# Optimization experiments

Hardware: AMD Instinct MI355X
Metric: run time of the kernel (lower is better)

## Reference

```python
import jax, jax.numpy as jnp
import numpy as np

N_NODES = 50000
N_EDGES = 800000
IN_F = 128
OUT_F = 128

def setup_inputs() -> dict:
    key = jax.random.key(0)
    k1, k2, k3, k4, k5, k6 = jax.random.split(key, 6)
    x = jax.random.normal(k1, (N_NODES, IN_F), dtype=jnp.float32)
    edge_row = jax.random.randint(k2, (N_EDGES,), 0, N_NODES, dtype=jnp.int32)
    edge_col = jax.random.randint(k3, (N_EDGES,), 0, N_NODES, dtype=jnp.int32)
    edge_val = jax.random.uniform(k4, (N_EDGES,), dtype=jnp.float32)
    stdv = 1.0 / np.sqrt(OUT_F)
    weight = jax.random.uniform(k5, (IN_F, OUT_F), minval=-stdv, maxval=stdv, dtype=jnp.float32)
    bias_param = jax.random.uniform(k6, (OUT_F,), minval=-stdv, maxval=stdv, dtype=jnp.float32)
    return {"x": x, "edge_row": edge_row, "edge_col": edge_col,
            "edge_val": edge_val, "weight": weight, "bias_param": bias_param}

def reference(x, edge_row, edge_col, edge_val, weight, bias_param):
    # support = X @ W  (dense GEMM)
    support = jnp.matmul(x, weight)                      # [N, out_f]
    # out = spmm(adj, support): gather source rows, scale by edge value,
    # scatter-add into destination rows (COO SpMM)
    msgs = edge_val[:, None] * support[edge_col]         # [E, out_f]
    out = jax.ops.segment_sum(msgs, edge_row, num_segments=N_NODES)
    return out + bias_param
```

## Files before the change

kernel.cpp:

```cpp
#include <hip/hip_runtime.h>

#define IN_F 128
#define OUT_F 128
#define BROWS 64
#define BCAP  2048
#define NBMAX 1024

typedef __attribute__((ext_vector_type(8))) short short8;
typedef __attribute__((ext_vector_type(4))) float floatx4;

__device__ __forceinline__ short f2bf(float f) {
  union { float f; unsigned u; } v; v.f = f;
  unsigned u = v.u;
  unsigned r = (u + 0x7fffu + ((u >> 16) & 1u)) >> 16;
  return (short)r;
}
__device__ __forceinline__ float bflo(unsigned u) { return __uint_as_float(u << 16); }
__device__ __forceinline__ float bfhi(unsigned u) { return __uint_as_float(u & 0xffff0000u); }

__global__ __launch_bounds__(256) void prep_wt(const float* __restrict__ w,
                                               short* __restrict__ wt) {
  int i = blockIdx.x * 256 + threadIdx.x;
  int n = i >> 7, k = i & 127;
  wt[i] = f2bf(w[k * 128 + n]);
}

__global__ __launch_bounds__(256) void gemm_mfma(const float* __restrict__ x,
                                                 const short* __restrict__ wt,
                                                 unsigned short* __restrict__ sup,
                                                 int n) {
  const int w    = threadIdx.x >> 6;
  const int lane = threadIdx.x & 63;
  const int m    = lane & 15;
  const int q    = lane >> 4;
  const int row  = blockIdx.x * 64 + w * 16 + m;

  floatx4 acc[8];
#pragma unroll
  for (int t = 0; t < 8; ++t) acc[t] = (floatx4)(0.f);

#pragma unroll
  for (int kk = 0; kk < 4; ++kk) {
    short8 a;
    if (row < n) {
      const float4* px = (const float4*)(x + (size_t)row * IN_F + kk * 32 + q * 8);
      float4 lo = px[0], hi = px[1];
      a[0] = f2bf(lo.x); a[1] = f2bf(lo.y); a[2] = f2bf(lo.z); a[3] = f2bf(lo.w);
      a[4] = f2bf(hi.x); a[5] = f2bf(hi.y); a[6] = f2bf(hi.z); a[7] = f2bf(hi.w);
    } else {
      a = (short8)(0);
    }
#pragma unroll
    for (int t = 0; t < 8; ++t) {
      short8 b = *(const short8*)(wt + (size_t)(16 * t + m) * 128 + kk * 32 + q * 8);
      acc[t] = __builtin_amdgcn_mfma_f32_16x16x32_bf16(a, b, acc[t], 0, 0, 0);
    }
  }

#pragma unroll
  for (int r = 0; r < 4; ++r) {
    int row_out = blockIdx.x * 64 + w * 16 + q * 4 + r;
    if (row_out < n) {
#pragma unroll
      for (int t = 0; t < 8; ++t) {
        sup[(size_t)row_out * OUT_F + 16 * t + m] = (unsigned short)f2bf(acc[t][r]);
      }
    }
  }
}

__global__ __launch_bounds__(256) void init_cursor(int* __restrict__ cursor, int nb) {
  int b = blockIdx.x * 256 + threadIdx.x;
  if (b < nb) cursor[b] = b * BCAP;
}

__global__ __launch_bounds__(256) void bin_edges(const int* __restrict__ erow,
                                                 const int* __restrict__ ecol,
                                                 const float* __restrict__ eval_,
                                                 int* __restrict__ cursor,
                                                 int2* __restrict__ slab,
                                                 int n_edges, int nb) {
  __shared__ int lhist[NBMAX];
  const int t = threadIdx.x;
  for (int b = t; b < nb; b += 256) lhist[b] = 0;
  __syncthreads();

  const int base = blockIdx.x * 4096;
  int meta[16], col[16]; float val[16];
#pragma unroll
  for (int i = 0; i < 16; ++i) {
    int e = base + i * 256 + t;
    meta[i] = -1;
    if (e < n_edges) {
      int r  = erow[e];
      col[i] = ecol[e];
      val[i] = eval_[e];
      int b = r >> 6, rl = r & 63;
      int rank = atomicAdd(&lhist[b], 1);
      meta[i] = (b << 18) | (rl << 12) | rank;
    }
  }
  __syncthreads();

  for (int b = t; b < nb; b += 256) {
    int c = lhist[b];
    lhist[b] = c ? atomicAdd(&cursor[b], c) : 0;
  }
  __syncthreads();

#pragma unroll
  for (int i = 0; i < 16; ++i) {
    if (meta[i] >= 0) {
      int b = meta[i] >> 18, rl = (meta[i] >> 12) & 63, rank = meta[i] & 0xfff;
      int pos = lhist[b] + rank;
      if (pos < (b + 1) * BCAP)
        slab[pos] = make_int2(col[i] | (rl << 16), __float_as_int(val[i]));
    }
  }
}

__global__ __launch_bounds__(256) void spmm_sorted(const int* __restrict__ cursor,
                                                   const int2* __restrict__ slab,
                                                   const uint4* __restrict__ supv,
                                                   const float* __restrict__ bias,
                                                   float* __restrict__ out,
                                                   int n_nodes) {
  __shared__ int2 srec[BCAP];
  __shared__ int  roff[BROWS + 1];
  __shared__ int  rcur[BROWS];
  const int t = threadIdx.x, b = blockIdx.x;
  const int start = b * BCAP;
  const int cnt = min(cursor[b] - start, BCAP);
  const int w = t >> 6, lane = t & 63;

  if (t < BROWS) rcur[t] = 0;
  __syncthreads();
  for (int i = t; i < cnt; i += 256)
    atomicAdd(&rcur[(slab[start + i].x >> 16) & 63], 1);
  __syncthreads();
  if (w == 0) {
    int inc = rcur[lane];
    #pragma unroll
    for (int d = 1; d < 64; d <<= 1) {
      int u = __shfl_up(inc, d);
      if (lane >= d) inc += u;
    }
    roff[lane + 1] = inc;
    if (lane == 0) roff[0] = 0;
  }
  __syncthreads();
  if (t < BROWS) rcur[t] = roff[t];
  __syncthreads();
  for (int i = t; i < cnt; i += 256) {
    int2 r = slab[start + i];
    int p = atomicAdd(&rcur[(r.x >> 16) & 63], 1);
    srec[p] = r;
  }
  __syncthreads();

  const int g = lane >> 4, s = lane & 15;
  const float4* bp = (const float4*)bias + s * 2;
  const float4 b0 = bp[0], b1 = bp[1];

  for (int it = 0; it < 4; ++it) {
    const int rl = w * 16 + it * 4 + g;
    const int s0 = roff[rl];
    const int c  = roff[rl + 1] - s0;
    int mx = max(c, __shfl_xor(c, 16));
    mx = max(mx, __shfl_xor(mx, 32));

    float a0 = 0.f, a1 = 0.f, a2 = 0.f, a3 = 0.f,
          a4 = 0.f, a5 = 0.f, a6 = 0.f, a7 = 0.f;

    int2 rec0 = make_int2(0, 0), rec1 = make_int2(0, 0);
    if (0 < c) rec0 = srec[s0];
    if (1 < c) rec1 = srec[s0 + 1];
    uint4 sv0 = supv[(size_t)(rec0.x & 0xffff) * 16 + s];
    uint4 sv1 = supv[(size_t)(rec1.x & 0xffff) * 16 + s];

    for (int j = 0; j < mx; ++j) {
      int2 rec2 = make_int2(0, 0);
      if (j + 2 < c) rec2 = srec[s0 + j + 2];
      uint4 sv2 = supv[(size_t)(rec2.x & 0xffff) * 16 + s];
      float v = (j < c) ? __int_as_float(rec0.y) : 0.f;
      a0 = fmaf(v, bflo(sv0.x), a0);
      a1 = fmaf(v, bfhi(sv0.x), a1);
      a2 = fmaf(v, bflo(sv0.y), a2);
      a3 = fmaf(v, bfhi(sv0.y), a3);
      a4 = fmaf(v, bflo(sv0.z), a4);
      a5 = fmaf(v, bfhi(sv0.z), a5);
      a6 = fmaf(v, bflo(sv0.w), a6);
      a7 = fmaf(v, bfhi(sv0.w), a7);
      rec0 = rec1; rec1 = rec2; sv0 = sv1; sv1 = sv2;
    }

    const int row = b * BROWS + rl;
    if (row < n_nodes) {
      float4* op = (float4*)(out + (size_t)row * OUT_F + s * 8);
      op[0] = make_float4(a0 + b0.x, a1 + b0.y, a2 + b0.z, a3 + b0.w);
      op[1] = make_float4(a4 + b1.x, a5 + b1.y, a6 + b1.z, a7 + b1.w);
    }
  }
}

extern "C" void kernel_launch(void* const* d_in, const int* in_sizes, int n_in,
                              void* d_out, int out_size, void* d_ws, size_t ws_size,
                              hipStream_t stream) {
  const float* x     = (const float*)d_in[0];
  const int*   erow  = (const int*)d_in[1];
  const int*   ecol  = (const int*)d_in[2];
  const float* eval_ = (const float*)d_in[3];
  const float* w     = (const float*)d_in[4];
  const float* bias  = (const float*)d_in[5];
  float* out = (float*)d_out;

  const int n_nodes = in_sizes[0] / IN_F;
  const int n_edges = in_sizes[1];
  const int nb = (n_nodes + BROWS - 1) / BROWS;

  char* ws = (char*)d_ws;
  size_t off = 0;
  auto carve = [&](size_t bytes) { void* p = ws + off; off = (off + bytes + 255) & ~(size_t)255; return p; };
  unsigned short* sup = (unsigned short*)carve((size_t)n_nodes * OUT_F * sizeof(unsigned short));
  short* wt           = (short*)carve((size_t)IN_F * OUT_F * sizeof(short));
  int*   cursor       = (int*)  carve((size_t)nb * sizeof(int));
  int2*  slab         = (int2*) carve((size_t)nb * BCAP * sizeof(int2));

  prep_wt<<<(IN_F * OUT_F) / 256, 256, 0, stream>>>(w, wt);
  gemm_mfma<<<(n_nodes + 63) / 64, 256, 0, stream>>>(x, wt, sup, n_nodes);
  init_cursor<<<(nb + 255) / 256, 256, 0, stream>>>(cursor, nb);
  bin_edges<<<(n_edges + 4095) / 4096, 256, 0, stream>>>(erow, ecol, eval_, cursor, slab,
                                                         n_edges, nb);
  spmm_sorted<<<nb, 256, 0, stream>>>(cursor, slab, (const uint4*)sup, bias, out, n_nodes);
}
```

Baseline: 152.0 us.

## Fuse cursor init into weight prep, coalesce GEMM stores, sort rows by degree

Folds the cursor-initialisation kernel into the weight-transpose kernel, removing one launch. The GEMM epilogue now stages bf16 results in a padded shared tile and writes 16-byte coalesced rows instead of scattered 2-byte stores. The SpMM kernel bitonic-sorts the block's 64 rows by edge count and assigns sorted rows to 16-lane groups, so the four rows in each wavefront have similar degrees and the per-wavefront loop bound wastes fewer iterations. The costs are extra shared memory and a small sort step per block.

```diff
diff --git a/kernel.cpp b/kernel.cpp
--- a/kernel.cpp
+++ b/kernel.cpp
@@ -18,17 +18,20 @@
 __device__ __forceinline__ float bflo(unsigned u) { return __uint_as_float(u << 16); }
 __device__ __forceinline__ float bfhi(unsigned u) { return __uint_as_float(u & 0xffff0000u); }
 
-__global__ __launch_bounds__(256) void prep_wt(const float* __restrict__ w,
-                                               short* __restrict__ wt) {
+__global__ __launch_bounds__(256) void prep_all(const float* __restrict__ w,
+                                                short* __restrict__ wt,
+                                                int* __restrict__ cursor, int nb) {
   int i = blockIdx.x * 256 + threadIdx.x;
   int n = i >> 7, k = i & 127;
   wt[i] = f2bf(w[k * 128 + n]);
+  if (i < nb) cursor[i] = i * BCAP;
 }
 
 __global__ __launch_bounds__(256) void gemm_mfma(const float* __restrict__ x,
                                                  const short* __restrict__ wt,
                                                  unsigned short* __restrict__ sup,
                                                  int n) {
+  __shared__ __align__(16) unsigned short stile[4][16 * 136];
   const int w    = threadIdx.x >> 6;
   const int lane = threadIdx.x & 63;
   const int m    = lane & 15;
@@ -58,20 +61,20 @@
   }
 
 #pragma unroll
-  for (int r = 0; r < 4; ++r) {
-    int row_out = blockIdx.x * 64 + w * 16 + q * 4 + r;
-    if (row_out < n) {
-#pragma unroll
-      for (int t = 0; t < 8; ++t) {
-        sup[(size_t)row_out * OUT_F + 16 * t + m] = (unsigned short)f2bf(acc[t][r]);
-      }
-    }
-  }
-}
-
-__global__ __launch_bounds__(256) void init_cursor(int* __restrict__ cursor, int nb) {
-  int b = blockIdx.x * 256 + threadIdx.x;
-  if (b < nb) cursor[b] = b * BCAP;
+  for (int r = 0; r < 4; ++r)
+#pragma unroll
+    for (int t = 0; t < 8; ++t)
+      stile[w][(q * 4 + r) * 136 + 16 * t + m] = (unsigned short)f2bf(acc[t][r]);
+
+#pragma unroll
+  for (int p = 0; p < 4; ++p) {
+    int row_l = p * 4 + (lane >> 4);
+    int row_g = blockIdx.x * 64 + w * 16 + row_l;
+    if (row_g < n) {
+      uint4 v = *(const uint4*)&stile[w][row_l * 136 + (lane & 15) * 8];
+      *(uint4*)(sup + (size_t)row_g * OUT_F + (lane & 15) * 8) = v;
+    }
+  }
 }
 
 __global__ __launch_bounds__(256) void bin_edges(const int* __restrict__ erow,
@@ -128,6 +131,7 @@
   __shared__ int2 srec[BCAP];
   __shared__ int  roff[BROWS + 1];
   __shared__ int  rcur[BROWS];
+  __shared__ int  srow[BROWS];
   const int t = threadIdx.x, b = blockIdx.x;
   const int start = b * BCAP;
   const int cnt = min(cursor[b] - start, BCAP);
@@ -139,14 +143,27 @@
     atomicAdd(&rcur[(slab[start + i].x >> 16) & 63], 1);
   __syncthreads();
   if (w == 0) {
-    int inc = rcur[lane];
-    #pragma unroll
+    int c = rcur[lane];
+    int inc = c;
+#pragma unroll
     for (int d = 1; d < 64; d <<= 1) {
       int u = __shfl_up(inc, d);
       if (lane >= d) inc += u;
     }
     roff[lane + 1] = inc;
     if (lane == 0) roff[0] = 0;
+    int key = (c << 6) | lane;
+#pragma unroll
+    for (int k = 2; k <= 64; k <<= 1) {
+#pragma unroll
+      for (int j = k >> 1; j > 0; j >>= 1) {
+        int other = __shfl_xor(key, j);
+        bool keep_min = (((lane & k) == 0) == ((lane & j) == 0));
+        int mn = min(key, other), mx = max(key, other);
+        key = keep_min ? mn : mx;
+      }
+    }
+    srow[lane] = key & 63;
   }
   __syncthreads();
   if (t < BROWS) rcur[t] = roff[t];
@@ -163,7 +180,7 @@
   const float4 b0 = bp[0], b1 = bp[1];
 
   for (int it = 0; it < 4; ++it) {
-    const int rl = w * 16 + it * 4 + g;
+    const int rl = srow[it * 16 + w * 4 + g];
     const int s0 = roff[rl];
     const int c  = roff[rl + 1] - s0;
     int mx = max(c, __shfl_xor(c, 16));
@@ -226,9 +243,8 @@
   int*   cursor       = (int*)  carve((size_t)nb * sizeof(int));
   int2*  slab         = (int2*) carve((size_t)nb * BCAP * sizeof(int2));
 
-  prep_wt<<<(IN_F * OUT_F) / 256, 256, 0, stream>>>(w, wt);
+  prep_all<<<64, 256, 0, stream>>>(w, wt, cursor, nb);
   gemm_mfma<<<(n_nodes + 63) / 64, 256, 0, stream>>>(x, wt, sup, n_nodes);
-  init_cursor<<<(nb + 255) / 256, 256, 0, stream>>>(cursor, nb);
   bin_edges<<<(n_edges + 4095) / 4096, 256, 0, stream>>>(erow, ecol, eval_, cursor, slab,
                                                          n_edges, nb);
   spmm_sorted<<<nb, 256, 0, stream>>>(cursor, slab, (const uint4*)sup, bias, out, n_nodes);
```

New measurement: 149.7 us. About the same (-1.5%).
